# Kernel tuning notes

Hardware: AMD Instinct MI355X
Metric: run time of the kernel (lower is better)

## Reference

```python
import jax, jax.numpy as jnp
import numpy as np

G, B, S, D = 4, 1, 1024, 2048   # num_gpus (chunks), batch, seq_local, model dim
H, DH = 32, 64                  # heads, dim_head; inner_dim = H*DH = D
EPS = 1e-6
NEG = -1e30                     # finite stand-in for -inf lse init (grad-safe)


def setup_inputs() -> dict:
    key = jax.random.key(0)
    ks = jax.random.split(key, 8)
    wsc = 1.0 / np.sqrt(D)  # keep pre-softmax logits in a sane range
    return {
        'x':  jax.random.normal(ks[0], (G, B, S, D), jnp.float32),
        'Wq': jax.random.normal(ks[1], (D, D), jnp.float32) * wsc,
        'bq': jnp.zeros((D,), jnp.float32),
        'Wk': jax.random.normal(ks[2], (D, D), jnp.float32) * wsc,
        'bk': jnp.zeros((D,), jnp.float32),
        'Wv': jax.random.normal(ks[3], (D, D), jnp.float32) * wsc,
        'bv': jnp.zeros((D,), jnp.float32),
        'qn_w': jnp.ones((D,), jnp.float32),
        'kn_w': jnp.ones((D,), jnp.float32),
        'Wo': jax.random.normal(ks[4], (D, D), jnp.float32) * wsc,
        'bo': jnp.zeros((D,), jnp.float32),
    }


def _rms_norm(t, w):
    return t * jax.lax.rsqrt(jnp.mean(t * t, axis=-1, keepdims=True) + EPS) * w


def reference(x, Wq, bq, Wk, bk, Wv, bv, qn_w, kn_w, Wo, bo):
    # x: [G, B, S, D] -- per-'GPU' sequence chunks
    q = _rms_norm(x @ Wq.T + bq, qn_w)
    k = _rms_norm(x @ Wk.T + bk, kn_w)
    v = x @ Wv.T + bv
    split = lambda t: t.reshape(G, B, S, H, DH).transpose(0, 1, 3, 2, 4)  # [G,B,H,S,DH]
    q, k, v = split(q), split(k), split(v)
    scale = 1.0 / np.sqrt(DH)

    out = jnp.zeros_like(q)
    lse = jnp.full((G, B, H, S, 1), NEG, q.dtype)
    kc, vc = k, v
    # Ring: each chunk attends to the visiting K/V chunk with online softmax.
    for _ in range(G):
        scores = jnp.einsum('gbhqd,gbhkd->gbhqk', q, kc) * scale
        m = scores.max(axis=-1, keepdims=True)
        e = jnp.exp(scores - m)
        ssum = e.sum(axis=-1, keepdims=True)
        chunk_lse = m + jnp.log(ssum)
        chunk_out = jnp.einsum('gbhqk,gbhkd->gbhqd', e / ssum, vc)
        new_lse = jnp.logaddexp(lse, chunk_lse)
        out = out * jnp.exp(lse - new_lse) + chunk_out * jnp.exp(chunk_lse - new_lse)
        lse = new_lse
        # rotate K/V around the ring: device i receives from device i-1
        kc = jnp.roll(kc, 1, axis=0)
        vc = jnp.roll(vc, 1, axis=0)

    o = out.transpose(0, 1, 3, 2, 4).reshape(G, B, S, H * DH)
    return o @ Wo.T + bo
```

## Files before the change

kernel.cpp:

```cpp
#include <hip/hip_runtime.h>

typedef __bf16 bf16x8 __attribute__((ext_vector_type(8)));
typedef float f32x4 __attribute__((ext_vector_type(4)));
typedef float f32x16 __attribute__((ext_vector_type(16)));
typedef unsigned short u16x8 __attribute__((ext_vector_type(8)));
typedef unsigned u32x2 __attribute__((ext_vector_type(2)));
typedef unsigned u32x4 __attribute__((ext_vector_type(4)));

__device__ __forceinline__ unsigned short f2bf(float f) {
  union { float f; unsigned u; } v; v.f = f;
  unsigned r = (v.u + 0x7fffu + ((v.u >> 16) & 1u)) >> 16;
  return (unsigned short)r;
}
__device__ __forceinline__ float bf2f(unsigned short s) {
  union { unsigned u; float f; } v; v.u = ((unsigned)s) << 16;
  return v.f;
}

#define GLD16(g, l)                                                        \
  __builtin_amdgcn_global_load_lds(                                        \
      (const __attribute__((address_space(1))) void*)(g),                  \
      (__attribute__((address_space(3))) void*)(l), 16, 0, 0)

__device__ __forceinline__ int swzc(int row, int colel) {
  return colel ^ ((((row & 7) ^ ((row >> 3) & 7)) & 7) << 3);
}

__device__ __forceinline__ u32x2 plswap(unsigned a, unsigned b) {
  return __builtin_amdgcn_permlane32_swap(a, b, false, false);
}
__device__ __forceinline__ float pair_sum(float x) {
  u32x2 r = plswap(__float_as_uint(x), __float_as_uint(x));
  return __uint_as_float(r.x) + __uint_as_float(r.y);
}
__device__ __forceinline__ unsigned cvtpk(float a, float b) {
  unsigned r;
  asm("v_cvt_pk_bf16_f32 %0, %1, %2" : "=v"(r) : "v"(a), "v"(b));
  return r;
}

__global__ __launch_bounds__(256) void cast_bf16_kernel(
    const float* __restrict__ in, unsigned short* __restrict__ out, int n4) {
  int i = blockIdx.x * 256 + threadIdx.x;
  int stride = gridDim.x * 256;
  for (; i < n4; i += stride) {
    float4 f = reinterpret_cast<const float4*>(in)[i];
    ushort4 s;
    s.x = f2bf(f.x); s.y = f2bf(f.y); s.z = f2bf(f.z); s.w = f2bf(f.w);
    reinterpret_cast<ushort4*>(out)[i] = s;
  }
}

__global__ __launch_bounds__(256) void cast_w4_kernel(
    const float* __restrict__ w0, const float* __restrict__ w1,
    const float* __restrict__ w2, const float* __restrict__ w3,
    unsigned short* __restrict__ o0, unsigned short* __restrict__ o1,
    unsigned short* __restrict__ o2, unsigned short* __restrict__ o3) {
  int i = blockIdx.x * 256 + threadIdx.x;
  int stride = gridDim.x * 256;
  for (; i < 4194304; i += stride) {
    int sel = i >> 20;
    const float* src = sel == 0 ? w0 : sel == 1 ? w1 : sel == 2 ? w2 : w3;
    unsigned short* dst = sel == 0 ? o0 : sel == 1 ? o1 : sel == 2 ? o2 : o3;
    int j = i & 1048575;
    float4 f = reinterpret_cast<const float4*>(src)[j];
    ushort4 s;
    s.x = f2bf(f.x); s.y = f2bf(f.y); s.z = f2bf(f.z); s.w = f2bf(f.w);
    reinterpret_cast<ushort4*>(dst)[j] = s;
  }
}

#define STG_A(STEP, KS, BUF)                                                   \
  GLD16(Ag + (size_t)(row0 + st_row0) * 2048 + (STEP) * 64 + (KS) * 32 +       \
            st_col0,                                                           \
        &ls[((BUF) * 2 + (KS)) * 4096 + (wid * 2) * 512]);                     \
  GLD16(Ag + (size_t)(row0 + st_row1) * 2048 + (STEP) * 64 + (KS) * 32 +       \
            st_col1,                                                           \
        &ls[((BUF) * 2 + (KS)) * 4096 + (wid * 2 + 1) * 512]);

#define STG_B(STEP, KS, BUF)                                                   \
  GLD16(Bg + (size_t)(col0 + st_row0) * 2048 + (STEP) * 64 + (KS) * 32 +       \
            st_col0,                                                           \
        &ls[16384 + ((BUF) * 2 + (KS)) * 4096 + (wid * 2) * 512]);             \
  GLD16(Bg + (size_t)(col0 + st_row1) * 2048 + (STEP) * 64 + (KS) * 32 +       \
            st_col1,                                                           \
        &ls[16384 + ((BUF) * 2 + (KS)) * 4096 + (wid * 2 + 1) * 512]);

#define VM8 asm volatile("s_waitcnt vmcnt(8)" ::: "memory");
#define VM4 asm volatile("s_waitcnt vmcnt(4)" ::: "memory");
#define VM0 asm volatile("s_waitcnt vmcnt(0)" ::: "memory");

#define PHASE(BUF, KS, MQ, RB, STG, VMW)                                       \
  {                                                                            \
    af0 = *(const bf16x8*)&ls[((BUF) * 2 + (KS)) * 4096 + offA[(MQ) * 2 + 0]]; \
    af1 = *(const bf16x8*)&ls[((BUF) * 2 + (KS)) * 4096 + offA[(MQ) * 2 + 1]]; \
    if (RB) {                                                                  \
      bfr[0] = *(const bf16x8*)&ls[16384 + ((BUF) * 2 + (KS)) * 4096 + offB[0]]; \
      bfr[1] = *(const bf16x8*)&ls[16384 + ((BUF) * 2 + (KS)) * 4096 + offB[1]]; \
      bfr[2] = *(const bf16x8*)&ls[16384 + ((BUF) * 2 + (KS)) * 4096 + offB[2]]; \
      bfr[3] = *(const bf16x8*)&ls[16384 + ((BUF) * 2 + (KS)) * 4096 + offB[3]]; \
    }                                                                          \
    STG;                                                                       \
    __builtin_amdgcn_s_barrier();                                              \
    __builtin_amdgcn_s_setprio(1);                                             \
    acc[(MQ) * 2 + 0][0] = __builtin_amdgcn_mfma_f32_16x16x32_bf16(            \
        af0, bfr[0], acc[(MQ) * 2 + 0][0], 0, 0, 0);                           \
    acc[(MQ) * 2 + 0][1] = __builtin_amdgcn_mfma_f32_16x16x32_bf16(            \
        af0, bfr[1], acc[(MQ) * 2 + 0][1], 0, 0, 0);                           \
    acc[(MQ) * 2 + 0][2] = __builtin_amdgcn_mfma_f32_16x16x32_bf16(            \
        af0, bfr[2], acc[(MQ) * 2 + 0][2], 0, 0, 0);                           \
    acc[(MQ) * 2 + 0][3] = __builtin_amdgcn_mfma_f32_16x16x32_bf16(            \
        af0, bfr[3], acc[(MQ) * 2 + 0][3], 0, 0, 0);                           \
    acc[(MQ) * 2 + 1][0] = __builtin_amdgcn_mfma_f32_16x16x32_bf16(            \
        af1, bfr[0], acc[(MQ) * 2 + 1][0], 0, 0, 0);                           \
    acc[(MQ) * 2 + 1][1] = __builtin_amdgcn_mfma_f32_16x16x32_bf16(            \
        af1, bfr[1], acc[(MQ) * 2 + 1][1], 0, 0, 0);                           \
    acc[(MQ) * 2 + 1][2] = __builtin_amdgcn_mfma_f32_16x16x32_bf16(            \
        af1, bfr[2], acc[(MQ) * 2 + 1][2], 0, 0, 0);                           \
    acc[(MQ) * 2 + 1][3] = __builtin_amdgcn_mfma_f32_16x16x32_bf16(            \
        af1, bfr[3], acc[(MQ) * 2 + 1][3], 0, 0, 0);                           \
    __builtin_amdgcn_s_setprio(0);                                             \
    VMW;                                                                       \
    __builtin_amdgcn_s_barrier();                                              \
  }

template <int F32OUT>
__global__ __launch_bounds__(256, 2) void gemm8p(
    const unsigned short* __restrict__ Ag,
    const unsigned short* __restrict__ W0, const unsigned short* __restrict__ W1,
    const unsigned short* __restrict__ W2,
    const float* __restrict__ b0, const float* __restrict__ b1,
    const float* __restrict__ b2,
    void* __restrict__ C0, void* __restrict__ C1, void* __restrict__ C2) {
  extern __shared__ __align__(16) unsigned short ls[];

  const int lin = blockIdx.y * gridDim.x + blockIdx.x;
  const int cpx = (gridDim.x * gridDim.y) >> 3;
  const int swz = (lin & 7) * cpx + (lin >> 3);
  const int bx = swz % gridDim.x, by = swz / gridDim.x;

  const int gcol = bx * 128;
  const int sel = gcol >> 11;
  const unsigned short* Bg = sel == 0 ? W0 : sel == 1 ? W1 : W2;
  const float* bias = sel == 0 ? b0 : sel == 1 ? b1 : b2;
  void* Cp = sel == 0 ? C0 : sel == 1 ? C1 : C2;
  const int col0 = gcol & 2047;
  const int row0 = by * 128;

  const int tid = threadIdx.x, lane = tid & 63, wid = tid >> 6;
  const int l15 = lane & 15, l4 = lane >> 4;
  const int wm = wid >> 1, wn = wid & 1;

  const int ci0 = wid * 2, ci1 = wid * 2 + 1;
  const int st_row0 = ci0 * 16 + (lane >> 2);
  const int st_row1 = ci1 * 16 + (lane >> 2);
  const int sl2a = ((lane >> 2) & 3) ^ ((lane >> 4) & 3);
  const int st_col0 = (((lane & 3) ^ (sl2a ^ (ci0 & 3))) * 8);
  const int st_col1 = (((lane & 3) ^ (sl2a ^ (ci1 & 3))) * 8);

  const int lsel = (l15 & 3) ^ ((l15 >> 2) & 3);
  int offA[4], offB[4];
#pragma unroll
  for (int f = 0; f < 4; ++f)
    offA[f] = (wm * 64 + f * 16 + l15) * 32 + ((l4 ^ lsel ^ (f & 3)) & 3) * 8;
#pragma unroll
  for (int ni = 0; ni < 4; ++ni)
    offB[ni] =
        (wn * 64 + ni * 16 + l15) * 32 + ((l4 ^ lsel ^ ((wn * 4 + ni) & 3)) & 3) * 8;

  f32x4 acc[4][4] = {};
  bf16x8 af0, af1, bfr[4];

  STG_A(0, 0, 0); STG_B(0, 0, 0);
  STG_A(0, 1, 0); STG_B(0, 1, 0);
  STG_A(1, 0, 1); STG_B(1, 0, 1);
  VM8;
  __builtin_amdgcn_s_barrier();

  for (int it = 0; it < 15; ++it) {
    const int sE = 2 * it, sO = sE + 1;
    PHASE(0, 0, 0, 1, STG_A(sO, 1, 1), );
    PHASE(0, 0, 1, 0, STG_B(sO, 1, 1), VM8);
    PHASE(0, 1, 0, 1, STG_A(sE + 2, 0, 0), );
    PHASE(0, 1, 1, 0, STG_B(sE + 2, 0, 0), VM8);
    PHASE(1, 0, 0, 1, STG_A(sE + 2, 1, 0), );
    PHASE(1, 0, 1, 0, STG_B(sE + 2, 1, 0), VM8);
    PHASE(1, 1, 0, 1, STG_A(sO + 2, 0, 1), );
    PHASE(1, 1, 1, 0, STG_B(sO + 2, 0, 1), VM8);
  }
  PHASE(0, 0, 0, 1, STG_A(31, 1, 1), );
  PHASE(0, 0, 1, 0, STG_B(31, 1, 1), VM8);
  PHASE(0, 1, 0, 1, , );
  PHASE(0, 1, 1, 0, , VM4);
  PHASE(1, 0, 0, 1, , );
  PHASE(1, 0, 1, 0, , VM0);
  PHASE(1, 1, 0, 1, , );
  PHASE(1, 1, 1, 0, , );

#pragma unroll
  for (int f = 0; f < 4; ++f)
#pragma unroll
    for (int ni = 0; ni < 4; ++ni)
#pragma unroll
      for (int r = 0; r < 4; ++r) {
        int row = row0 + wm * 64 + f * 16 + l4 * 4 + r;
        int col = col0 + wn * 64 + ni * 16 + l15;
        float v = acc[f][ni][r] + bias[col];
        if (F32OUT)
          ((float*)Cp)[(size_t)row * 2048 + col] = v;
        else
          ((unsigned short*)Cp)[(size_t)row * 2048 + col] = f2bf(v);
      }
}

__global__ __launch_bounds__(256) void rmsnorm2_kernel(
    unsigned short* __restrict__ Qb, unsigned short* __restrict__ Kb,
    const float* __restrict__ qw, const float* __restrict__ kw) {
  const int row = blockIdx.x;
  unsigned short* p;
  const float* w;
  if (row < 4096) { p = Qb + (size_t)row * 2048; w = qw; }
  else            { p = Kb + (size_t)(row - 4096) * 2048; w = kw; }
  const int tid = threadIdx.x;
  u16x8 v = *(const u16x8*)&p[tid * 8];
  float f[8];
  float ss = 0.f;
#pragma unroll
  for (int j = 0; j < 8; ++j) { f[j] = bf2f(v[j]); ss += f[j] * f[j]; }
#pragma unroll
  for (int m = 1; m < 64; m <<= 1) ss += __shfl_xor(ss, m, 64);
  __shared__ float red[4];
  const int wid = tid >> 6, lane = tid & 63;
  if (lane == 0) red[wid] = ss;
  __syncthreads();
  float tot = red[0] + red[1] + red[2] + red[3];
  float rs = rsqrtf(tot * (1.0f / 2048.0f) + 1e-6f);
  u16x8 o;
#pragma unroll
  for (int j = 0; j < 8; ++j) o[j] = f2bf(f[j] * rs * w[tid * 8 + j]);
  *(u16x8*)&p[tid * 8] = o;
}

__global__ __launch_bounds__(256, 4) void flash_attn(
    const unsigned short* __restrict__ Q, const unsigned short* __restrict__ K,
    const unsigned short* __restrict__ V, unsigned short* __restrict__ O) {
  __shared__ unsigned short Ks[2][64 * 64];
  __shared__ unsigned short Vs[2][64 * 64];
  const int bid = blockIdx.x;
  const int sw = (bid & 7) * 128 + (bid >> 3);
  const int h = sw >> 5;
  const int q0 = (sw & 31) * 128;
  const int tid = threadIdx.x, lane = tid & 63, wid = tid >> 6;
  const int l31 = lane & 31, hi = lane >> 5;

  const int kr0 = wid * 16 + (lane >> 3);
  const int kc0 = (lane & 7) * 8;
  const int vkey = (tid & 31) * 2;
  const int vd0 = (tid >> 5) * 8;

  const float QSCALE = 0.125f * 1.44269504f;
  bf16x8 qf[4];
  {
    const int qrow = q0 + wid * 32 + l31;
#pragma unroll
    for (int kt = 0; kt < 4; ++kt) {
      bf16x8 raw = *(const bf16x8*)&Q[(size_t)qrow * 2048 + h * 64 + kt * 16 + hi * 8];
#pragma unroll
      for (int j = 0; j < 8; ++j) qf[kt][j] = (__bf16)((float)raw[j] * QSCALE);
    }
  }

  int off[2][4];
#pragma unroll
  for (int kb = 0; kb < 2; ++kb) {
    const int row = kb * 32 + l31;
    const int sl = (((row & 7) ^ ((row >> 3) & 7)) & 7) << 3;
#pragma unroll
    for (int kt = 0; kt < 4; ++kt)
      off[kb][kt] = row * 64 + ((kt * 16 + hi * 8) ^ sl);
  }

  float l_r = 0.f;
  f32x16 oa[2] = {};

  u16x8 kreg0, kreg1, vreg0, vreg1;
  auto loadKV = [&](int kt0) {
    kreg0 = *(const u16x8*)&K[(size_t)(kt0 + kr0) * 2048 + h * 64 + kc0];
    kreg1 = *(const u16x8*)&K[(size_t)(kt0 + kr0 + 8) * 2048 + h * 64 + kc0];
    vreg0 = *(const u16x8*)&V[(size_t)(kt0 + vkey) * 2048 + h * 64 + vd0];
    vreg1 = *(const u16x8*)&V[(size_t)(kt0 + vkey + 1) * 2048 + h * 64 + vd0];
  };
  auto writeKV = [&](int b) {
    *(u16x8*)&Ks[b][kr0 * 64 + swzc(kr0, kc0)] = kreg0;
    *(u16x8*)&Ks[b][(kr0 + 8) * 64 + swzc(kr0 + 8, kc0)] = kreg1;
#pragma unroll
    for (int d = 0; d < 8; ++d) {
      int row = vd0 + d;
      *(unsigned*)&Vs[b][row * 64 + swzc(row, vkey)] =
          (unsigned)vreg0[d] | ((unsigned)vreg1[d] << 16);
    }
  };

  loadKV(0);
  writeKV(0);
  __syncthreads();

  for (int t = 0; t < 64; ++t) {
    const int cur = t & 1;
    if (t < 63) loadKV((t + 1) * 64);

    const unsigned short* Kc = Ks[cur];
    const unsigned short* Vc = Vs[cur];

    f32x16 st[2];
    __builtin_amdgcn_s_setprio(1);
#pragma unroll
    for (int kb = 0; kb < 2; ++kb) {
      f32x16 a = {};
#pragma unroll
      for (int kt = 0; kt < 4; ++kt) {
        bf16x8 kf = *(const bf16x8*)&Kc[off[kb][kt]];
        a = __builtin_amdgcn_mfma_f32_32x32x16_bf16(kf, qf[kt], a, 0, 0, 0);
      }
      st[kb] = a;
    }
    __builtin_amdgcn_s_setprio(0);

    unsigned pk[16];
    float s0 = 0.f, s1 = 0.f, s2 = 0.f, s3 = 0.f;
#pragma unroll
    for (int kb = 0; kb < 2; ++kb)
#pragma unroll
      for (int j = 0; j < 8; ++j) {
        float pa = __builtin_amdgcn_exp2f(st[kb][2 * j]);
        float pb = __builtin_amdgcn_exp2f(st[kb][2 * j + 1]);
        if ((j & 3) == 0) s0 += pa + pb;
        else if ((j & 3) == 1) s1 += pa + pb;
        else if ((j & 3) == 2) s2 += pa + pb;
        else s3 += pa + pb;
        pk[kb * 8 + j] = cvtpk(pa, pb);
      }
    l_r += (s0 + s1) + (s2 + s3);

    bf16x8 pfrag[4];
#pragma unroll
    for (int kt = 0; kt < 4; ++kt) {
      u32x2 sa = plswap(pk[4 * kt + 0], pk[4 * kt + 2]);
      u32x2 sb = plswap(pk[4 * kt + 1], pk[4 * kt + 3]);
      union { u32x4 u; bf16x8 b; } w;
      w.u.x = sa.x; w.u.y = sb.x; w.u.z = sa.y; w.u.w = sb.y;
      pfrag[kt] = w.b;
    }

    __builtin_amdgcn_s_setprio(1);
#pragma unroll
    for (int dv = 0; dv < 2; ++dv) {
#pragma unroll
      for (int kt = 0; kt < 4; ++kt) {
        bf16x8 vf = *(const bf16x8*)&Vc[off[dv][kt]];
        oa[dv] = __builtin_amdgcn_mfma_f32_32x32x16_bf16(vf, pfrag[kt], oa[dv], 0, 0, 0);
      }
    }
    __builtin_amdgcn_s_setprio(0);

    if (t < 63) {
      writeKV(cur ^ 1);
      __syncthreads();
    }
  }

  const float inv = 1.0f / pair_sum(l_r);
  const int qrow = q0 + wid * 32 + l31;
#pragma unroll
  for (int dv = 0; dv < 2; ++dv)
#pragma unroll
    for (int tq = 0; tq < 4; ++tq) {
      unsigned w0 = cvtpk(oa[dv][4 * tq + 0] * inv, oa[dv][4 * tq + 1] * inv);
      unsigned w1 = cvtpk(oa[dv][4 * tq + 2] * inv, oa[dv][4 * tq + 3] * inv);
      int dh = 32 * dv + 8 * tq + 4 * hi;
      u32x2 w2 = {w0, w1};
      *(u32x2*)&O[(size_t)qrow * 2048 + h * 64 + dh] = w2;
    }
}

extern "C" void kernel_launch(void* const* d_in, const int* in_sizes, int n_in,
                              void* d_out, int out_size, void* d_ws, size_t ws_size,
                              hipStream_t stream) {
  const float* x  = (const float*)d_in[0];
  const float* Wq = (const float*)d_in[1];
  const float* bq = (const float*)d_in[2];
  const float* Wk = (const float*)d_in[3];
  const float* bk = (const float*)d_in[4];
  const float* Wv = (const float*)d_in[5];
  const float* bv = (const float*)d_in[6];
  const float* qn = (const float*)d_in[7];
  const float* kn = (const float*)d_in[8];
  const float* Wo = (const float*)d_in[9];
  const float* bo = (const float*)d_in[10];

  char* w = (char*)d_ws;
  unsigned short* Xbf = (unsigned short*)(w);
  unsigned short* Wqb = (unsigned short*)(w + 16777216);
  unsigned short* Wkb = (unsigned short*)(w + 25165824);
  unsigned short* Wvb = (unsigned short*)(w + 33554432);
  unsigned short* Wob = (unsigned short*)(w + 41943040);
  unsigned short* Qb  = (unsigned short*)(w + 50331648);
  unsigned short* Kb  = (unsigned short*)(w + 67108864);
  unsigned short* Vb  = (unsigned short*)(w + 83886080);
  unsigned short* Ob  = Xbf;

  cast_bf16_kernel<<<1024, 256, 0, stream>>>(x, Xbf, 8388608 / 4);
  cast_w4_kernel<<<2048, 256, 0, stream>>>(Wq, Wk, Wv, Wo, Wqb, Wkb, Wvb, Wob);

  gemm8p<0><<<dim3(48, 32), 256, 65536, stream>>>(
      Xbf, Wqb, Wkb, Wvb, bq, bk, bv, Qb, Kb, Vb);

  rmsnorm2_kernel<<<8192, 256, 0, stream>>>(Qb, Kb, qn, kn);

  flash_attn<<<1024, 256, 0, stream>>>(Qb, Kb, Vb, Ob);

  gemm8p<1><<<dim3(16, 32), 256, 65536, stream>>>(
      Ob, Wob, Wob, Wob, bo, bo, bo, d_out, d_out, d_out);
}
```

Before: 392.0 us.

## Process two 32-row query tiles per wave in flash attention to reuse K/V fragments

Each wave now handles 64 query rows instead of 32, so the block covers 256 queries, and each K and V fragment read from LDS feeds two MFMA chains. The grid halves to 512 blocks and launch bounds drop to 2 blocks per CU to leave room for the doubled accumulators. The aim is to halve LDS reads and K/V global traffic per query. The costs are higher register pressure, fewer resident waves to hide latency, and fewer blocks (512) to spread across the CUs.

```diff
diff --git a/kernel.cpp b/kernel.cpp
--- a/kernel.cpp
+++ b/kernel.cpp
@@ -241,15 +241,15 @@
   *(u16x8*)&p[tid * 8] = o;
 }
 
-__global__ __launch_bounds__(256, 4) void flash_attn(
+__global__ __launch_bounds__(256, 2) void flash_attn(
     const unsigned short* __restrict__ Q, const unsigned short* __restrict__ K,
     const unsigned short* __restrict__ V, unsigned short* __restrict__ O) {
   __shared__ unsigned short Ks[2][64 * 64];
   __shared__ unsigned short Vs[2][64 * 64];
   const int bid = blockIdx.x;
-  const int sw = (bid & 7) * 128 + (bid >> 3);
-  const int h = sw >> 5;
-  const int q0 = (sw & 31) * 128;
+  const int sw = (bid & 7) * 64 + (bid >> 3);
+  const int h = sw >> 4;
+  const int q0 = (sw & 15) * 256;
   const int tid = threadIdx.x, lane = tid & 63, wid = tid >> 6;
   const int l31 = lane & 31, hi = lane >> 5;
 
@@ -259,14 +259,18 @@
   const int vd0 = (tid >> 5) * 8;
 
   const float QSCALE = 0.125f * 1.44269504f;
-  bf16x8 qf[4];
+  bf16x8 qf0[4], qf1[4];
   {
-    const int qrow = q0 + wid * 32 + l31;
+    const int qr0 = q0 + wid * 64 + l31;
 #pragma unroll
     for (int kt = 0; kt < 4; ++kt) {
-      bf16x8 raw = *(const bf16x8*)&Q[(size_t)qrow * 2048 + h * 64 + kt * 16 + hi * 8];
-#pragma unroll
-      for (int j = 0; j < 8; ++j) qf[kt][j] = (__bf16)((float)raw[j] * QSCALE);
+      bf16x8 r0 = *(const bf16x8*)&Q[(size_t)qr0 * 2048 + h * 64 + kt * 16 + hi * 8];
+      bf16x8 r1 = *(const bf16x8*)&Q[(size_t)(qr0 + 32) * 2048 + h * 64 + kt * 16 + hi * 8];
+#pragma unroll
+      for (int j = 0; j < 8; ++j) {
+        qf0[kt][j] = (__bf16)((float)r0[j] * QSCALE);
+        qf1[kt][j] = (__bf16)((float)r1[j] * QSCALE);
+      }
     }
   }
 
@@ -280,8 +284,8 @@
       off[kb][kt] = row * 64 + ((kt * 16 + hi * 8) ^ sl);
   }
 
-  float l_r = 0.f;
-  f32x16 oa[2] = {};
+  float l0 = 0.f, l1 = 0.f;
+  f32x16 oa0[2] = {}, oa1[2] = {};
 
   u16x8 kreg0, kreg1, vreg0, vreg1;
   auto loadKV = [&](int kt0) {
@@ -312,54 +316,95 @@
     const unsigned short* Kc = Ks[cur];
     const unsigned short* Vc = Vs[cur];
 
-    f32x16 st[2];
+    bf16x8 kf[2][4];
+#pragma unroll
+    for (int kb = 0; kb < 2; ++kb)
+#pragma unroll
+      for (int kt = 0; kt < 4; ++kt)
+        kf[kb][kt] = *(const bf16x8*)&Kc[off[kb][kt]];
+
+    f32x16 st0[2], st1[2];
     __builtin_amdgcn_s_setprio(1);
 #pragma unroll
     for (int kb = 0; kb < 2; ++kb) {
       f32x16 a = {};
 #pragma unroll
-      for (int kt = 0; kt < 4; ++kt) {
-        bf16x8 kf = *(const bf16x8*)&Kc[off[kb][kt]];
-        a = __builtin_amdgcn_mfma_f32_32x32x16_bf16(kf, qf[kt], a, 0, 0, 0);
-      }
-      st[kb] = a;
+      for (int kt = 0; kt < 4; ++kt)
+        a = __builtin_amdgcn_mfma_f32_32x32x16_bf16(kf[kb][kt], qf0[kt], a, 0, 0, 0);
+      st0[kb] = a;
+    }
+#pragma unroll
+    for (int kb = 0; kb < 2; ++kb) {
+      f32x16 a = {};
+#pragma unroll
+      for (int kt = 0; kt < 4; ++kt)
+        a = __builtin_amdgcn_mfma_f32_32x32x16_bf16(kf[kb][kt], qf1[kt], a, 0, 0, 0);
+      st1[kb] = a;
     }
     __builtin_amdgcn_s_setprio(0);
 
-    unsigned pk[16];
-    float s0 = 0.f, s1 = 0.f, s2 = 0.f, s3 = 0.f;
-#pragma unroll
-    for (int kb = 0; kb < 2; ++kb)
-#pragma unroll
-      for (int j = 0; j < 8; ++j) {
-        float pa = __builtin_amdgcn_exp2f(st[kb][2 * j]);
-        float pb = __builtin_amdgcn_exp2f(st[kb][2 * j + 1]);
-        if ((j & 3) == 0) s0 += pa + pb;
-        else if ((j & 3) == 1) s1 += pa + pb;
-        else if ((j & 3) == 2) s2 += pa + pb;
-        else s3 += pa + pb;
-        pk[kb * 8 + j] = cvtpk(pa, pb);
-      }
-    l_r += (s0 + s1) + (s2 + s3);
-
-    bf16x8 pfrag[4];
+    unsigned pk0[16], pk1[16];
+    {
+      float s0 = 0.f, s1 = 0.f, s2 = 0.f, s3 = 0.f;
+#pragma unroll
+      for (int kb = 0; kb < 2; ++kb)
+#pragma unroll
+        for (int j = 0; j < 8; ++j) {
+          float pa = __builtin_amdgcn_exp2f(st0[kb][2 * j]);
+          float pb = __builtin_amdgcn_exp2f(st0[kb][2 * j + 1]);
+          if ((j & 3) == 0) s0 += pa + pb;
+          else if ((j & 3) == 1) s1 += pa + pb;
+          else if ((j & 3) == 2) s2 += pa + pb;
+          else s3 += pa + pb;
+          pk0[kb * 8 + j] = cvtpk(pa, pb);
+        }
+      l0 += (s0 + s1) + (s2 + s3);
+    }
+    {
+      float s0 = 0.f, s1 = 0.f, s2 = 0.f, s3 = 0.f;
+#pragma unroll
+      for (int kb = 0; kb < 2; ++kb)
+#pragma unroll
+        for (int j = 0; j < 8; ++j) {
+          float pa = __builtin_amdgcn_exp2f(st1[kb][2 * j]);
+          float pb = __builtin_amdgcn_exp2f(st1[kb][2 * j + 1]);
+          if ((j & 3) == 0) s0 += pa + pb;
+          else if ((j & 3) == 1) s1 += pa + pb;
+          else if ((j & 3) == 2) s2 += pa + pb;
+          else s3 += pa + pb;
+          pk1[kb * 8 + j] = cvtpk(pa, pb);
+        }
+      l1 += (s0 + s1) + (s2 + s3);
+    }
+
+    bf16x8 pfrag0[4], pfrag1[4];
 #pragma unroll
     for (int kt = 0; kt < 4; ++kt) {
-      u32x2 sa = plswap(pk[4 * kt + 0], pk[4 * kt + 2]);
-      u32x2 sb = plswap(pk[4 * kt + 1], pk[4 * kt + 3]);
+      u32x2 sa = plswap(pk0[4 * kt + 0], pk0[4 * kt + 2]);
+      u32x2 sb = plswap(pk0[4 * kt + 1], pk0[4 * kt + 3]);
       union { u32x4 u; bf16x8 b; } w;
       w.u.x = sa.x; w.u.y = sb.x; w.u.z = sa.y; w.u.w = sb.y;
-      pfrag[kt] = w.b;
+      pfrag0[kt] = w.b;
+      u32x2 sc = plswap(pk1[4 * kt + 0], pk1[4 * kt + 2]);
+      u32x2 sd = plswap(pk1[4 * kt + 1], pk1[4 * kt + 3]);
+      union { u32x4 u; bf16x8 b; } w2;
+      w2.u.x = sc.x; w2.u.y = sd.x; w2.u.z = sc.y; w2.u.w = sd.y;
+      pfrag1[kt] = w2.b;
     }
 
     __builtin_amdgcn_s_setprio(1);
 #pragma unroll
     for (int dv = 0; dv < 2; ++dv) {
-#pragma unroll
-      for (int kt = 0; kt < 4; ++kt) {
-        bf16x8 vf = *(const bf16x8*)&Vc[off[dv][kt]];
-        oa[dv] = __builtin_amdgcn_mfma_f32_32x32x16_bf16(vf, pfrag[kt], oa[dv], 0, 0, 0);
-      }
+      bf16x8 vf[4];
+#pragma unroll
+      for (int kt = 0; kt < 4; ++kt)
+        vf[kt] = *(const bf16x8*)&Vc[off[dv][kt]];
+#pragma unroll
+      for (int kt = 0; kt < 4; ++kt)
+        oa0[dv] = __builtin_amdgcn_mfma_f32_32x32x16_bf16(vf[kt], pfrag0[kt], oa0[dv], 0, 0, 0);
+#pragma unroll
+      for (int kt = 0; kt < 4; ++kt)
+        oa1[dv] = __builtin_amdgcn_mfma_f32_32x32x16_bf16(vf[kt], pfrag1[kt], oa1[dv], 0, 0, 0);
     }
     __builtin_amdgcn_s_setprio(0);
 
@@ -369,17 +414,22 @@
     }
   }
 
-  const float inv = 1.0f / pair_sum(l_r);
-  const int qrow = q0 + wid * 32 + l31;
+  const float inv0 = 1.0f / pair_sum(l0);
+  const float inv1 = 1.0f / pair_sum(l1);
+  const int qr0 = q0 + wid * 64 + l31;
 #pragma unroll
   for (int dv = 0; dv < 2; ++dv)
 #pragma unroll
     for (int tq = 0; tq < 4; ++tq) {
-      unsigned w0 = cvtpk(oa[dv][4 * tq + 0] * inv, oa[dv][4 * tq + 1] * inv);
-      unsigned w1 = cvtpk(oa[dv][4 * tq + 2] * inv, oa[dv][4 * tq + 3] * inv);
       int dh = 32 * dv + 8 * tq + 4 * hi;
-      u32x2 w2 = {w0, w1};
-      *(u32x2*)&O[(size_t)qrow * 2048 + h * 64 + dh] = w2;
+      unsigned a0 = cvtpk(oa0[dv][4 * tq + 0] * inv0, oa0[dv][4 * tq + 1] * inv0);
+      unsigned a1 = cvtpk(oa0[dv][4 * tq + 2] * inv0, oa0[dv][4 * tq + 3] * inv0);
+      u32x2 wa = {a0, a1};
+      *(u32x2*)&O[(size_t)qr0 * 2048 + h * 64 + dh] = wa;
+      unsigned b0 = cvtpk(oa1[dv][4 * tq + 0] * inv1, oa1[dv][4 * tq + 1] * inv1);
+      unsigned b1 = cvtpk(oa1[dv][4 * tq + 2] * inv1, oa1[dv][4 * tq + 3] * inv1);
+      u32x2 wb = {b0, b1};
+      *(u32x2*)&O[(size_t)(qr0 + 32) * 2048 + h * 64 + dh] = wb;
     }
 }
 
@@ -417,7 +467,7 @@
 
   rmsnorm2_kernel<<<8192, 256, 0, stream>>>(Qb, Kb, qn, kn);
 
-  flash_attn<<<1024, 256, 0, stream>>>(Qb, Kb, Vb, Ob);
+  flash_attn<<<512, 256, 0, stream>>>(Qb, Kb, Vb, Ob);
 
   gemm8p<1><<<dim3(16, 32), 256, 65536, stream>>>(
       Ob, Wob, Wob, Wob, bo, bo, bo, d_out, d_out, d_out);
```

Result: faster. 359.8 us (-8.2%).
